# Kernel tuning notes

Hardware: AMD Instinct MI355X
Metric: run time of the kernel (lower is better)

Reference implementation:

```python
import jax, jax.numpy as jnp
import numpy as np

K = 16                 # hardcoded k in KL_divergence default
TYPICAL_CRLB = 0.15 * 100 / 10   # = 1.5, sigma used in KL divergence


def setup_inputs() -> dict:
    key = jax.random.key(0)
    k1, k2 = jax.random.split(key)
    N = 8192
    ch1 = jax.random.normal(k1, (N, 2), dtype=jnp.float32)
    ch2 = jax.random.normal(k2, (N, 2), dtype=jnp.float32)
    # Polynomial layer parameters, exactly as in __init__ (identity-ish map)
    M1 = jnp.array([[0.0, 0.0], [1.0, 0.0]], dtype=jnp.float32)
    M2 = jnp.array([[0.0, 1.0], [0.0, 0.0]], dtype=jnp.float32)
    return {"ch1": ch1, "ch2": ch2, "M1": M1, "M2": M2}


def _polynomial(x, M1, M2):
    # out[:,0] = sum_ij M1[i,j] * x1^i * x2^j ; out[:,1] analog with M2 (m=2)
    x1, x2 = x[:, 0], x[:, 1]
    pi = jnp.stack([jnp.ones_like(x1), x1], axis=1)          # [N,2] -> x1^i
    pj = jnp.stack([jnp.ones_like(x2), x2], axis=1)          # [N,2] -> x2^j
    B = pi[:, :, None] * pj[:, None, :]                      # [N,2,2] basis x1^i*x2^j
    y1 = jnp.einsum('nij,ij->n', B, M1)
    y2 = jnp.einsum('nij,ij->n', B, M2)
    return jnp.stack([y1, y2], axis=1)                       # [N,2]


def reference(ch1, ch2, M1, M2):
    N = ch1.shape[0]
    ch2m = _polynomial(ch2, M1, M2)

    # --- KNN ---
    diff = ch1[None, :, :] - ch2m[:, None, :]                # [N2, N1, 2]
    distances = diff * diff                                  # squared per-coord dists
    abs_distances = jnp.sum(distances, axis=2)               # [N2, N1]
    # top_k of negated transposed distances: for each ch1 point, k nearest ch2m
    _, idx = jax.lax.top_k(-abs_distances.T, K)              # [N1, K] indices into ch2 axis
    # Faithful reproduction of the original index construction:
    # idx is flattened row-major ([N,K]); indx1 flattens a [K,N] arange-broadcast,
    # so the second coordinate at flat position t is t % N.
    flat_a = idx.reshape(-1)                                 # [N*K] indexes axis 0 (ch2)
    flat_b = jnp.tile(jnp.arange(N), K)                      # [N*K] indexes axis 1 (ch1)
    knn = distances[flat_a, flat_b].reshape(K, N, 2)         # [K, N, 2]

    # --- KL divergence ---
    sigma2 = TYPICAL_CRLB
    D_KL = 0.5 * jnp.sum(knn / (sigma2 ** 2), axis=2)        # [K, N]

    # --- Rel entropy ---
    expD = jnp.sum(jnp.exp(-D_KL), axis=0) / N               # [N]
    mask = expD != 0.0                                       # tf boolean_mask of nonzeros
    safe = jnp.where(mask, expD, 1.0)
    return -jnp.sum(jnp.where(mask, jnp.log(safe), 0.0))
```

## Files before the change

### kernel.cpp

```cpp
#include <hip/hip_runtime.h>
#include <math.h>
#include <stdint.h>

#define K_NN 16
#define NPTS 8192
#define NR 32
#define PADN (NPTS + 64)

static __device__ __constant__ float d_bt[33] = {
    -3.4028235e38f,
    -1.8627318f, -1.5341205f, -1.3180109f, -1.1503494f, -1.0100762f,
    -0.8871466f, -0.7764218f, -0.6744898f, -0.5791322f, -0.4887764f,
    -0.4022501f, -0.3186394f, -0.2372021f, -0.1573107f, -0.0784124f,
     0.0f,
     0.0784124f,  0.1573107f,  0.2372021f,  0.3186394f,  0.4022501f,
     0.4887764f,  0.5791322f,  0.6744898f,  0.7764218f,  0.8871466f,
     1.0100762f,  1.1503494f,  1.3180109f,  1.5341205f,  1.8627318f,
     3.4028235e38f
};

__device__ __forceinline__ int rowOf(const float* bt, float y) {
    int c = 0;
    c += (y >= bt[c + 16]) ? 16 : 0;
    c += (y >= bt[c + 8])  ? 8  : 0;
    c += (y >= bt[c + 4])  ? 4  : 0;
    c += (y >= bt[c + 2])  ? 2  : 0;
    c += (y >= bt[c + 1])  ? 1  : 0;
    return c;
}

__global__ __launch_bounds__(1024) void kq_fused(const float* __restrict__ ch1,
                                                 const float* __restrict__ ch2,
                                                 const float* __restrict__ M1,
                                                 const float* __restrict__ M2,
                                                 int* __restrict__ midx,
                                                 float* __restrict__ out) {
    __shared__ __align__(16) float2 shp[PADN];
    __shared__ int h[NR];
    __shared__ int offs[NR];
    __shared__ int rs[NR + 1];
    __shared__ float bt[33];

    const int tid  = threadIdx.x;
    const int lane = tid & 63;
    const int w    = tid >> 6;
    const int qg   = blockIdx.x * 16 + w;

    if (blockIdx.x == 0 && tid == 0) out[0] = 0.0f;

    if (tid < 33) bt[tid] = d_bt[tid];
    if (tid < NR) h[tid] = 0;
    const float inf = __int_as_float(0x7F800000);
    for (int i = tid; i < PADN; i += 1024) shp[i] = make_float2(inf, inf);
    __syncthreads();

    const float a0 = M1[0], a1 = M1[1], a2 = M1[2], a3 = M1[3];
    const float b0 = M2[0], b1 = M2[1], b2 = M2[2], b3 = M2[3];
    const float4* __restrict__ g4 = (const float4*)ch2;

    float2 pts[8];
    int rw[8];
#pragma unroll
    for (int e = 0; e < 4; ++e) {
        float4 v = g4[e * 1024 + tid];
        pts[2 * e]     = make_float2(a0 + a1 * v.y + v.x * (a2 + a3 * v.y),
                                     b0 + b1 * v.y + v.x * (b2 + b3 * v.y));
        pts[2 * e + 1] = make_float2(a0 + a1 * v.w + v.z * (a2 + a3 * v.w),
                                     b0 + b1 * v.w + v.z * (b2 + b3 * v.w));
    }
#pragma unroll
    for (int p = 0; p < 8; ++p) {
        rw[p] = rowOf(bt, pts[p].y);
        atomicAdd(&h[rw[p]], 1);
    }
    __syncthreads();

    if (tid == 0) {
        int run = 0;
        for (int r = 0; r < NR; ++r) {
            offs[r] = run;
            rs[r] = run;
            run += (h[r] + 1) & ~1;
        }
        rs[NR] = run;
    }
    __syncthreads();

#pragma unroll
    for (int p = 0; p < 8; ++p) {
        int gi = 2 * ((p >> 1) * 1024 + tid) + (p & 1);
        int pos = atomicAdd(&offs[rw[p]], 1);
        unsigned ux = (__float_as_uint(pts[p].x) & ~0x7Fu) | ((unsigned)gi >> 6);
        unsigned uy = (__float_as_uint(pts[p].y) & ~0x3Fu) | ((unsigned)gi & 63u);
        shp[pos] = make_float2(__uint_as_float(ux), __uint_as_float(uy));
    }
    __syncthreads();

    int rsv = rs[lane < 33 ? lane : 0];
    int btb = __float_as_int(d_bt[lane < 33 ? lane : 0]);

    const float qx = ch1[2 * qg + 0];
    const float qy = ch1[2 * qg + 1];
    const int own = rowOf(d_bt, qy);

    unsigned key = 0xFFFFFFFFu;
    unsigned thr = 0xFFFFFFFFu;
    bool first = true;

#define SCAN_ROW(R)                                                            \
    {                                                                          \
        int lo = __builtin_amdgcn_readlane(rsv, (R));                          \
        int hi = __builtin_amdgcn_readlane(rsv, (R) + 1);       \
        for (int base = lo; base < hi; base += 128) {                          \
            int i0 = base + 2 * lane;                                          \
            int ii = min(i0, hi - 2);                         \
            float4 cc = *(const float4*)&shp[ii];                              \
            bool p0 = i0 < hi;                                                 \
            bool p1 = i0 + 1 < hi;                                             \
            float dx0 = qx - cc.x, dy0 = qy - cc.y;                            \
            float dx1 = qx - cc.z, dy1 = qy - cc.w;                            \
            unsigned u0 = p0 ? __float_as_uint(dx0 * dx0 + dy0 * dy0)          \
                             : 0xFFFFFFFFu;                                    \
            unsigned u1 = p1 ? __float_as_uint(dx1 * dx1 + dy1 * dy1)          \
                             : 0xFFFFFFFFu;                                    \
            if (first) {                                                       \
                first = false;                                                 \
                unsigned mn = min(u0, u1);                                     \
                mn = min(mn, (unsigned)__shfl_xor((int)mn, 1, 64));            \
                mn = min(mn, (unsigned)__shfl_xor((int)mn, 2, 64));            \
                unsigned mx = mn;                                              \
                mx = max(mx, (unsigned)__shfl_xor((int)mx, 4, 64));            \
                mx = max(mx, (unsigned)__shfl_xor((int)mx, 8, 64));            \
                mx = max(mx, (unsigned)__shfl_xor((int)mx, 16, 64));           \
                mx = max(mx, (unsigned)__shfl_xor((int)mx, 32, 64));           \
                thr = mx | 0x1FFFu;                                            \
            }                                                                  \
            unsigned id0 = ((__float_as_uint(cc.x) & 0x7Fu) << 6)              \
                         | (__float_as_uint(cc.y) & 0x3Fu);                    \
            unsigned id1 = ((__float_as_uint(cc.z) & 0x7Fu) << 6)              \
                         | (__float_as_uint(cc.w) & 0x3Fu);                    \
            unsigned nk0 = (u0 & 0xFFFFE000u) | id0;                           \
            unsigned nk1 = (u1 & 0xFFFFE000u) | id1;                           \
            unsigned long long m0 = __ballot(u0 <= thr);                       \
            unsigned long long m1 = __ballot(u1 <= thr);                       \
            while (m0) {                                                       \
                int l = __ffsll(m0) - 1;                                       \
                m0 &= m0 - 1;                                                  \
                unsigned snk = (unsigned)__builtin_amdgcn_readlane((int)nk0, l);\
                unsigned up = (unsigned)__builtin_amdgcn_update_dpp(           \
                    0, (int)key, 0x111, 0xF, 0xF, false);       \
                bool c1 = snk < key;                                           \
                unsigned nv = (snk < up) ? up : snk;                           \
                key = c1 ? nv : key;                                           \
            }                                                                  \
            while (m1) {                                                       \
                int l = __ffsll(m1) - 1;                                       \
                m1 &= m1 - 1;                                                  \
                unsigned snk = (unsigned)__builtin_amdgcn_readlane((int)nk1, l);\
                unsigned up = (unsigned)__builtin_amdgcn_update_dpp(           \
                    0, (int)key, 0x111, 0xF, 0xF, false);                      \
                bool c1 = snk < key;                                           \
                unsigned nv = (snk < up) ? up : snk;                           \
                key = c1 ? nv : key;                                           \
            }                                                                  \
            thr = (unsigned)__builtin_amdgcn_readlane((int)key, 15) | 0x1FFFu; \
        }                                                                      \
    }

    SCAN_ROW(own)

    bool loDone = false, hiDone = false;
    for (int d = 1; d < NR; ++d) {
        int rlo = own - d, rhi = own + d;
        if (!loDone) {
            if (rlo < 0) loDone = true;
            else {
                float band = qy - __uint_as_float(
                    __builtin_amdgcn_readlane(btb, rlo + 1));
                unsigned bb = __float_as_uint(band * band) & 0xFFFFE000u;
                if (bb > (thr & 0xFFFFE000u)) loDone = true;
                else SCAN_ROW(rlo)
            }
        }
        if (!hiDone) {
            if (rhi > NR - 1) hiDone = true;
            else {
                float band = __uint_as_float(
                    __builtin_amdgcn_readlane(btb, rhi)) - qy;
                unsigned bb = __float_as_uint(band * band) & 0xFFFFE000u;
                if (bb > (thr & 0xFFFFE000u)) hiDone = true;
                else SCAN_ROW(rhi)
            }
        }
        if (loDone && hiDone) break;
    }
#undef SCAN_ROW

    if (lane < K_NN)
        midx[qg * K_NN + lane] = (int)(key & 0x1FFFu);
}

__global__ __launch_bounds__(1024) void k3_final(const float* __restrict__ ch1,
                                                 const float* __restrict__ ch2,
                                                 const float* __restrict__ M1,
                                                 const float* __restrict__ M2,
                                                 const int* __restrict__ midx,
                                                 float* __restrict__ out, int N) {
    const float a0 = M1[0], a1 = M1[1], a2 = M1[2], a3 = M1[3];
    const float b0 = M2[0], b1 = M2[1], b2 = M2[2], b3 = M2[3];

    int t = blockIdx.x * 1024 + threadIdx.x;
    int n = t >> 4;
    int k = t & 15;
    int g = n >> 4;
    int r = n & 15;

    int j = k * (N / K_NN) + g;
    int a = midx[j * K_NN + r];
    float2 cp = ((const float2*)ch2)[a];
    float cx = a0 + a1 * cp.y + cp.x * (a2 + a3 * cp.y);
    float cy = b0 + b1 * cp.y + cp.x * (b2 + b3 * cp.y);
    float dx = ch1[2 * n + 0] - cx;
    float dy = ch1[2 * n + 1] - cy;
    float term = expf(-(dx * dx + dy * dy) * (1.0f / 4.5f));

#pragma unroll
    for (int off = 8; off; off >>= 1) term += __shfl_down(term, off, 16);

    float v = 0.0f;
    if (k == 0) {
        float expD = term / (float)N;
        v = (expD != 0.0f) ? logf(expD) : 0.0f;
    }
#pragma unroll
    for (int off = 32; off; off >>= 1) v += __shfl_down(v, off, 64);

    __shared__ float red[16];
    int lane = threadIdx.x & 63;
    int wv = threadIdx.x >> 6;
    if (lane == 0) red[wv] = v;
    __syncthreads();
    if (threadIdx.x == 0) {
        float s = 0.0f;
#pragma unroll
        for (int i = 0; i < 16; ++i) s += red[i];
        atomicAdd(out, -s);
    }
}

extern "C" void kernel_launch(void* const* d_in, const int* in_sizes, int n_in,
                              void* d_out, int out_size, void* d_ws, size_t ws_size,
                              hipStream_t stream) {
    const float* ch1 = (const float*)d_in[0];
    const float* ch2 = (const float*)d_in[1];
    const float* M1  = (const float*)d_in[2];
    const float* M2  = (const float*)d_in[3];
    float* out = (float*)d_out;
    const int N = in_sizes[0] / 2;

    int* midx = (int*)d_ws;

    kq_fused<<<N / 16, 1024, 0, stream>>>(ch1, ch2, M1, M2, midx, out);

    k3_final<<<(N * K_NN) / 1024, 1024, 0, stream>>>(ch1, ch2, M1, M2, midx, out, N);
}
```

Before: 87.89 us.

## Fuse KNN search and KL/log reduction into one kernel via query remapping

Merges the KNN kernel and the final entropy kernel into a single launch. Query rows are remapped (qg = w*512 + b) so that each block's 16 waves hold exactly the 16 neighbor rows that feed one group of 16 output points. This lets the exp, sum, log and atomic reduction happen in-block without writing the index buffer to global memory. The cost is a second kernel launch replaced by a memset, plus an extra block-level sync and a different query-to-block assignment that may change load balance.

```diff
diff --git a/kernel.cpp b/kernel.cpp
--- a/kernel.cpp
+++ b/kernel.cpp
@@ -29,24 +29,23 @@
     return c;
 }
 
-__global__ __launch_bounds__(1024) void kq_fused(const float* __restrict__ ch1,
-                                                 const float* __restrict__ ch2,
-                                                 const float* __restrict__ M1,
-                                                 const float* __restrict__ M2,
-                                                 int* __restrict__ midx,
-                                                 float* __restrict__ out) {
+__global__ __launch_bounds__(1024) void kall(const float* __restrict__ ch1,
+                                             const float* __restrict__ ch2,
+                                             const float* __restrict__ M1,
+                                             const float* __restrict__ M2,
+                                             float* __restrict__ out) {
     __shared__ __align__(16) float2 shp[PADN];
     __shared__ int h[NR];
     __shared__ int offs[NR];
     __shared__ int rs[NR + 1];
     __shared__ float bt[33];
+    __shared__ float red[16 * K_NN];
 
     const int tid  = threadIdx.x;
     const int lane = tid & 63;
     const int w    = tid >> 6;
-    const int qg   = blockIdx.x * 16 + w;
-
-    if (blockIdx.x == 0 && tid == 0) out[0] = 0.0f;
+    const int b    = blockIdx.x;
+    const int qg   = w * 512 + b;
 
     if (tid < 33) bt[tid] = d_bt[tid];
     if (tid < NR) h[tid] = 0;
@@ -196,55 +195,27 @@
     }
 #undef SCAN_ROW
 
-    if (lane < K_NN)
-        midx[qg * K_NN + lane] = (int)(key & 0x1FFFu);
-}
-
-__global__ __launch_bounds__(1024) void k3_final(const float* __restrict__ ch1,
-                                                 const float* __restrict__ ch2,
-                                                 const float* __restrict__ M1,
-                                                 const float* __restrict__ M2,
-                                                 const int* __restrict__ midx,
-                                                 float* __restrict__ out, int N) {
-    const float a0 = M1[0], a1 = M1[1], a2 = M1[2], a3 = M1[3];
-    const float b0 = M2[0], b1 = M2[1], b2 = M2[2], b3 = M2[3];
-
-    int t = blockIdx.x * 1024 + threadIdx.x;
-    int n = t >> 4;
-    int k = t & 15;
-    int g = n >> 4;
-    int r = n & 15;
-
-    int j = k * (N / K_NN) + g;
-    int a = midx[j * K_NN + r];
-    float2 cp = ((const float2*)ch2)[a];
-    float cx = a0 + a1 * cp.y + cp.x * (a2 + a3 * cp.y);
-    float cy = b0 + b1 * cp.y + cp.x * (b2 + b3 * cp.y);
-    float dx = ch1[2 * n + 0] - cx;
-    float dy = ch1[2 * n + 1] - cy;
-    float term = expf(-(dx * dx + dy * dy) * (1.0f / 4.5f));
-
-#pragma unroll
-    for (int off = 8; off; off >>= 1) term += __shfl_down(term, off, 16);
-
-    float v = 0.0f;
-    if (k == 0) {
-        float expD = term / (float)N;
-        v = (expD != 0.0f) ? logf(expD) : 0.0f;
-    }
-#pragma unroll
-    for (int off = 32; off; off >>= 1) v += __shfl_down(v, off, 64);
-
-    __shared__ float red[16];
-    int lane = threadIdx.x & 63;
-    int wv = threadIdx.x >> 6;
-    if (lane == 0) red[wv] = v;
-    __syncthreads();
-    if (threadIdx.x == 0) {
+    if (lane < K_NN) {
+        int a = (int)(key & 0x1FFFu);
+        float2 cp = ((const float2*)ch2)[a];
+        float cx = a0 + a1 * cp.y + cp.x * (a2 + a3 * cp.y);
+        float cy = b0 + b1 * cp.y + cp.x * (b2 + b3 * cp.y);
+        float2 q1 = ((const float2*)ch1)[16 * b + lane];
+        float dx = q1.x - cx;
+        float dy = q1.y - cy;
+        red[w * K_NN + lane] = expf(-(dx * dx + dy * dy) * (1.0f / 4.5f));
+    }
+    __syncthreads();
+
+    if (w == 0 && lane < K_NN) {
         float s = 0.0f;
 #pragma unroll
-        for (int i = 0; i < 16; ++i) s += red[i];
-        atomicAdd(out, -s);
+        for (int k = 0; k < 16; ++k) s += red[k * K_NN + lane];
+        float expD = s / (float)NPTS;
+        float v = (expD != 0.0f) ? logf(expD) : 0.0f;
+#pragma unroll
+        for (int off = 8; off; off >>= 1) v += __shfl_down(v, off, 16);
+        if (lane == 0) atomicAdd(out, -v);
     }
 }
 
@@ -256,11 +227,8 @@
     const float* M1  = (const float*)d_in[2];
     const float* M2  = (const float*)d_in[3];
     float* out = (float*)d_out;
-    const int N = in_sizes[0] / 2;
-
-    int* midx = (int*)d_ws;
-
-    kq_fused<<<N / 16, 1024, 0, stream>>>(ch1, ch2, M1, M2, midx, out);
-
-    k3_final<<<(N * K_NN) / 1024, 1024, 0, stream>>>(ch1, ch2, M1, M2, midx, out, N);
+
+    hipMemsetAsync(out, 0, sizeof(float), stream);
+
+    kall<<<NPTS / 16, 1024, 0, stream>>>(ch1, ch2, M1, M2, out);
 }
```

Measured after the change: 85.96 us. 1.02x faster.
